# Kernel optimization log

Hardware: AMD Instinct MI355X
Metric: run time of the kernel (lower is better)

Reference implementation:

```python
import jax, jax.numpy as jnp
import numpy as np

D = 384      # d_model
NH = 8       # num_heads
HW = 96      # spatial h = w
RATIOS = (4, 8, 16)


def _p2i(x):
    # (hg wg b) c h w -> b c (hg h) (wg w), hg=wg=2, b=1
    f, c, h, w = x.shape
    return x.reshape(2, 2, c, h, w).transpose(2, 0, 3, 1, 4).reshape(1, c, 2 * h, 2 * w)


def _i2p(x):
    # b c (hg h) (wg w) -> (hg wg b) c h w, hg=wg=2, b=1
    _, c, H2, W2 = x.shape
    h, w = H2 // 2, W2 // 2
    return x.reshape(c, 2, h, 2, w).transpose(1, 3, 0, 2, 4).reshape(4, c, h, w)


def _ln(x, g, b, eps=1e-5):
    m = x.mean(-1, keepdims=True)
    v = ((x - m) ** 2).mean(-1, keepdims=True)
    return (x - m) * jax.lax.rsqrt(v + eps) * g + b


def setup_inputs() -> dict:
    key = jax.random.key(0)
    ks = jax.random.split(key, 8)
    rn = lambda k, s: jax.random.normal(k, s, dtype=jnp.float32) * 0.02
    return {
        "x": jax.random.normal(ks[0], (5, D, HW, HW), dtype=jnp.float32),
        "sal_w": rn(ks[1], (1, D)),
        "sal_b": jnp.zeros((1,), jnp.float32),
        "attn_in_w": rn(ks[2], (4, 3 * D, D)),
        "attn_in_b": jnp.zeros((4, 3 * D), jnp.float32),
        "attn_out_w": rn(ks[3], (4, D, D)),
        "attn_out_b": jnp.zeros((4, D), jnp.float32),
        "w3": rn(ks[4], (2 * D, D)),
        "b3": jnp.zeros((2 * D,), jnp.float32),
        "w4": rn(ks[5], (D, 2 * D)),
        "b4": jnp.zeros((D,), jnp.float32),
        "g1": jnp.ones((D,), jnp.float32),
        "be1": jnp.zeros((D,), jnp.float32),
        "g2": jnp.ones((D,), jnp.float32),
        "be2": jnp.zeros((D,), jnp.float32),
    }


def reference(x, sal_w, sal_b, attn_in_w, attn_in_b, attn_out_w, attn_out_b,
              w3, b3, w4, b4, g1, be1, g2, be2):
    b, c, h, w = x.shape
    loc, glb = x[:4], x[4:5]                      # (4,c,h,w), (1,c,h,w)
    pg = _i2p(glb)                                # (4,c,h/2,w/2)

    tam = jax.nn.sigmoid(jnp.einsum('oc,chw->ohw', sal_w, glb[0]) + sal_b[:, None, None])  # (1,h,w)
    tam_up = jnp.repeat(jnp.repeat(tam, 2, axis=1), 2, axis=2)[None]                        # (1,1,2h,2w)
    loc = loc * _i2p(tam_up)                      # (4,c,h,w) * (4,1,h,w)

    # multi-ratio adaptive average pooling of patched global (sizes divide exactly)
    pools = []
    for r in RATIOS:
        th, tw = round(h / r), round(w / r)
        kh, kw = (h // 2) // th, (w // 2) // tw
        p = pg.reshape(4, c, th, kh, tw, kw).mean((3, 5))
        pools.append(p.reshape(4, c, th * tw))
    kv = jnp.concatenate(pools, axis=2).transpose(0, 2, 1)   # (4,S,c)

    q = loc.reshape(4, c, h * w).transpose(0, 2, 1)          # (4,L,c)

    # 4 independent MHA blocks, vectorized over the patch dim n
    dh = c // NH
    wq, wk, wv = attn_in_w[:, :c], attn_in_w[:, c:2 * c], attn_in_w[:, 2 * c:]
    bq, bk, bv = attn_in_b[:, :c], attn_in_b[:, c:2 * c], attn_in_b[:, 2 * c:]
    heads = lambda t: t.reshape(4, -1, NH, dh).transpose(0, 2, 1, 3)
    qh = heads(jnp.einsum('nlc,ndc->nld', q, wq) + bq[:, None, :])
    kh = heads(jnp.einsum('nsc,ndc->nsd', kv, wk) + bk[:, None, :])
    vh = heads(jnp.einsum('nsc,ndc->nsd', kv, wv) + bv[:, None, :])
    scores = jnp.einsum('nhld,nhsd->nhls', qh, kh) / jnp.sqrt(jnp.float32(dh))
    attn = jax.nn.softmax(scores, axis=-1)
    ao = jnp.einsum('nhls,nhsd->nhld', attn, vh).transpose(0, 2, 1, 3).reshape(4, -1, c)
    ao = jnp.einsum('nlc,ndc->nld', ao, attn_out_w) + attn_out_b[:, None, :]  # (4,L,c)
    outputs = ao.transpose(1, 0, 2)                                           # (L,4,c)

    # residual + FFN block (dropouts are identity in eval)
    src = loc.reshape(4, c, -1).transpose(2, 0, 1) + outputs                  # (L,4,c)
    src = _ln(src, g1, be1)
    hid = jax.nn.gelu(jnp.einsum('lnc,dc->lnd', src, w3) + b3, approximate=False)
    ff = jnp.einsum('lnd,cd->lnc', hid, w4) + b4
    src = _ln(src + ff, g2, be2)
    src = src.transpose(1, 2, 0).reshape(4, c, h, w)

    # nearest-downsample (factor 2) of stitched patches, add to global
    glb = glb + _p2i(src)[:, :, ::2, ::2]
    return jnp.concatenate([src, glb], axis=0)
```

## Files before the change

### kernel.cpp

```cpp
#include <hip/hip_runtime.h>

typedef __attribute__((ext_vector_type(8))) __bf16 bf16x8;
typedef __attribute__((ext_vector_type(4))) __bf16 bf16x4;
typedef __attribute__((ext_vector_type(4))) float f32x4;

__device__ __forceinline__ bf16x8 zero8() {
  bf16x8 z;
#pragma unroll
  for (int i = 0; i < 8; ++i) z[i] = (__bf16)0.f;
  return z;
}

__device__ __forceinline__ float wave_sum(float v) {
#pragma unroll
  for (int off = 1; off < 64; off <<= 1) v += __shfl_xor(v, off);
  return v;
}

__global__ __launch_bounds__(256) void k_cvt4(const float* __restrict__ a,
    const float* __restrict__ b, const float* __restrict__ c, const float* __restrict__ d,
    __bf16* __restrict__ oa, __bf16* __restrict__ ob, __bf16* __restrict__ oc,
    __bf16* __restrict__ od) {
  const int i = blockIdx.x * 256 + threadIdx.x;
  const float* src; __bf16* dst; int off;
  if (i < 442368)      { src = a; dst = oa; off = i; }
  else if (i < 589824) { src = b; dst = ob; off = i - 442368; }
  else if (i < 663552) { src = c; dst = oc; off = i - 589824; }
  else if (i < 737280) { src = d; dst = od; off = i - 663552; }
  else return;
  const f32x4 v = ((const f32x4*)src)[off];
  bf16x4 o;
#pragma unroll
  for (int e = 0; e < 4; ++e) o[e] = (__bf16)v[e];
  ((bf16x4*)dst)[off] = o;
}

__global__ __launch_bounds__(256) void k_tam(const float* __restrict__ x,
    const float* __restrict__ sal_w, const float* __restrict__ sal_b,
    float* __restrict__ tam) {
  const int lane = threadIdx.x & 63, w = threadIdx.x >> 6;
  const int pix = blockIdx.x * 64 + lane;
  const float* g = x + (size_t)4 * 384 * 9216;
  float acc = 0.f;
  for (int c = w * 96; c < w * 96 + 96; ++c)
    acc += sal_w[c] * g[(size_t)c * 9216 + pix];
  __shared__ float part[4][64];
  part[w][lane] = acc;
  __syncthreads();
  if (w == 0) {
    float v = part[0][lane] + part[1][lane] + part[2][lane] + part[3][lane] + sal_b[0];
    tam[pix] = 1.f / (1.f + __expf(-v));
  }
}

__global__ __launch_bounds__(256) void k_locscale(const float* __restrict__ x,
    const float* __restrict__ tam, __bf16* __restrict__ Q) {
  const int n = blockIdx.y;
  const int l0 = blockIdx.x * 64;
  const int tid = threadIdx.x;
  __shared__ float tile[64][69];
  const size_t bx = (size_t)n * 384 * 9216;
  const int a = n >> 1, b = n & 1;
  for (int c0 = 0; c0 < 384; c0 += 64) {
    if (c0) __syncthreads();
#pragma unroll
    for (int pass = 0; pass < 4; ++pass) {
      int cc = pass * 16 + (tid >> 4);
      int ll = (tid & 15) * 4;
      f32x4 v = *(const f32x4*)&x[bx + (size_t)(c0 + cc) * 9216 + l0 + ll];
#pragma unroll
      for (int e = 0; e < 4; ++e) tile[cc][ll + e] = v[e];
    }
    __syncthreads();
    const int ll = tid >> 2, c1 = (tid & 3) * 16;
    const int l = l0 + ll, i = l / 96, j = l % 96;
    const float tv = tam[(a * 48 + (i >> 1)) * 96 + b * 48 + (j >> 1)];
    const size_t orow = ((size_t)n * 9216 + l) * 384 + c0 + c1;
#pragma unroll
    for (int cc = 0; cc < 16; ++cc)
      Q[orow + cc] = (__bf16)(tile[c1 + cc][ll] * tv);
  }
}

__global__ __launch_bounds__(64) void k_pool(const float* __restrict__ x,
    __bf16* __restrict__ KV) {
  const int c = blockIdx.x, n = blockIdx.y;
  const int a = n >> 1, b = n & 1;
  const float* g = x + (size_t)(4 * 384 + c) * 9216;
  __shared__ float quad[48][48];
  const int t = threadIdx.x;
  for (int k = t; k < 2304; k += 64) {
    int i = k / 48, j = k % 48;
    quad[i][j] = g[(a * 48 + i) * 96 + b * 48 + j];
  }
  __syncthreads();
  for (int s = t; s < 768; s += 64) {
    float val = 0.f;
    if (s < 576) {
      int ti = s / 24, tj = s % 24;
#pragma unroll
      for (int di = 0; di < 2; ++di)
#pragma unroll
        for (int dj = 0; dj < 2; ++dj) val += quad[ti * 2 + di][tj * 2 + dj];
      val *= 0.25f;
    } else if (s < 720) {
      int q = s - 576; int ti = q / 12, tj = q % 12;
      for (int di = 0; di < 4; ++di)
        for (int dj = 0; dj < 4; ++dj) val += quad[ti * 4 + di][tj * 4 + dj];
      val *= (1.f / 16.f);
    } else if (s < 756) {
      int q = s - 720; int ti = q / 6, tj = q % 6;
      for (int di = 0; di < 8; ++di)
        for (int dj = 0; dj < 8; ++dj) val += quad[ti * 8 + di][tj * 8 + dj];
      val *= (1.f / 64.f);
    }
    KV[((size_t)n * 768 + s) * 384 + c] = (__bf16)val;
  }
}

template <int GELU>
__global__ __launch_bounds__(256) void k_gemm(const __bf16* __restrict__ A,
    const __bf16* __restrict__ B, const float* __restrict__ bias,
    __bf16* __restrict__ C, int K, long sA, long sB, long sBias, long sC,
    float scale) {
  const int z = blockIdx.z;
  A += (size_t)z * sA; B += (size_t)z * sB; bias += (size_t)z * sBias; C += (size_t)z * sC;
  const int m0 = blockIdx.y * 128, n0 = blockIdx.x * 128;
  const int N = gridDim.x * 128;
  __shared__ __bf16 As[128 * 64], Bs[128 * 64];
  const int tid = threadIdx.x, lane = tid & 63, w = tid >> 6;
  const int wm = w >> 1, wn = w & 1;
  const int li = lane & 15, gq = lane >> 4;
  const int lrow = lane >> 3, lcol = (lane & 7) * 8;
  f32x4 acc[4][4] = {};
  const int nk = K >> 6;
  for (int kt = 0; kt < nk; ++kt) {
    const int k0 = kt * 64;
#pragma unroll
    for (int i = 0; i < 4; ++i) {
      const int r0 = w * 32 + i * 8;
      const __bf16* ga = A + (size_t)(m0 + r0 + lrow) * K + k0 + lcol;
      const __bf16* gb = B + (size_t)(n0 + r0 + lrow) * K + k0 + lcol;
      __builtin_amdgcn_global_load_lds(
          (const __attribute__((address_space(1))) void*)ga,
          (__attribute__((address_space(3))) void*)&As[r0 * 64], 16, 0, 0);
      __builtin_amdgcn_global_load_lds(
          (const __attribute__((address_space(1))) void*)gb,
          (__attribute__((address_space(3))) void*)&Bs[r0 * 64], 16, 0, 0);
    }
    __syncthreads();
#pragma unroll
    for (int kk = 0; kk < 2; ++kk) {
      bf16x8 af[4], bfr[4];
#pragma unroll
      for (int f = 0; f < 4; ++f) {
        af[f] = *(const bf16x8*)&As[(wm * 64 + f * 16 + li) * 64 + kk * 32 + gq * 8];
        bfr[f] = *(const bf16x8*)&Bs[(wn * 64 + f * 16 + li) * 64 + kk * 32 + gq * 8];
      }
#pragma unroll
      for (int fm = 0; fm < 4; ++fm)
#pragma unroll
        for (int fn = 0; fn < 4; ++fn)
          acc[fm][fn] = __builtin_amdgcn_mfma_f32_16x16x32_bf16(af[fm], bfr[fn], acc[fm][fn], 0, 0, 0);
    }
    __syncthreads();
  }
  float bv[4];
#pragma unroll
  for (int fn = 0; fn < 4; ++fn) bv[fn] = bias[n0 + wn * 64 + fn * 16 + li];
#pragma unroll
  for (int fm = 0; fm < 4; ++fm) {
    const int row = m0 + wm * 64 + fm * 16 + gq * 4;
#pragma unroll
    for (int fn = 0; fn < 4; ++fn) {
      const int col = n0 + wn * 64 + fn * 16 + li;
#pragma unroll
      for (int r = 0; r < 4; ++r) {
        float v = (acc[fm][fn][r] + bv[fn]) * scale;
        if (GELU) v = 0.5f * v * (1.f + erff(v * 0.70710678118654752f));
        C[(size_t)(row + r) * N + col] = (__bf16)v;
      }
    }
  }
}

__global__ __launch_bounds__(256) void k_kmax(const __bf16* __restrict__ KVH,
    float* __restrict__ kmax) {
  const int nh = blockIdx.x, n = nh >> 3, h = nh & 7;
  const size_t bk = (size_t)n * 768 * 768 + h * 48;
  const int tid = threadIdx.x;
  float m = 0.f;
  for (int s = tid; s < 756; s += 256) {
    float a2 = 0.f;
#pragma unroll
    for (int ch = 0; ch < 6; ++ch) {
      bf16x8 kv = *(const bf16x8*)&KVH[bk + (size_t)s * 768 + ch * 8];
#pragma unroll
      for (int e = 0; e < 8; ++e) { const float f = (float)kv[e]; a2 += f * f; }
    }
    m = fmaxf(m, a2);
  }
#pragma unroll
  for (int off = 1; off < 64; off <<= 1) m = fmaxf(m, __shfl_xor(m, off));
  __shared__ float red[4];
  if ((tid & 63) == 0) red[tid >> 6] = m;
  __syncthreads();
  if (tid == 0) kmax[nh] = fmaxf(fmaxf(red[0], red[1]), fmaxf(red[2], red[3]));
}

__global__ __launch_bounds__(256) void k_vt(const __bf16* __restrict__ KVH,
    __bf16* __restrict__ VT) {
  const int nh = blockIdx.y, n = nh >> 3, h = nh & 7;
  const int s0 = blockIdx.x * 256;
  __shared__ __bf16 tile[48][264];
  const int tid = threadIdx.x;
  const size_t bv = (size_t)n * 768 * 768 + 384 + h * 48;
#pragma unroll
  for (int it = 0; it < 6; ++it) {
    const int task = tid + it * 256;
    const int s = task / 6, ch = task % 6;
    bf16x8 v = *(const bf16x8*)&KVH[bv + (size_t)(s0 + s) * 768 + ch * 8];
#pragma unroll
    for (int e = 0; e < 8; ++e) tile[ch * 8 + e][s] = v[e];
  }
  __syncthreads();
#pragma unroll
  for (int it = 0; it < 6; ++it) {
    const int task = tid + it * 256;
    const int d = task >> 5, so = (task & 31) * 8;
    bf16x8 v2 = *(const bf16x8*)&tile[d][so];
    *(bf16x8*)&VT[((size_t)nh * 48 + d) * 768 + s0 + so] = v2;
  }
}

__global__ __launch_bounds__(256) void k_attn(const __bf16* __restrict__ QH,
    const __bf16* __restrict__ KVH, const __bf16* __restrict__ VT,
    const float* __restrict__ kmax, __bf16* __restrict__ AO) {
  const int nh = blockIdx.y, n = nh >> 3, h = nh & 7;
  const int l0 = blockIdx.x * 64;
  const int tid = threadIdx.x, lane = tid & 63, w = tid >> 6;
  const int gq = lane >> 4, li = lane & 15;
  const int l0w = l0 + w * 16;
  __shared__ __bf16 Ks[64 * 64];
  __shared__ __bf16 Vs[48 * 64];
  __shared__ __bf16 P[4][16 * 68];
  __bf16* Pw = &P[w][0];
  const size_t bq = ((size_t)n * 9216) * 384 + h * 48;
  const size_t bk = (size_t)n * 768 * 768 + h * 48;
  const __bf16* vt = VT + (size_t)nh * 48 * 768;
  const int scol = 8 * ((lane & 7) ^ (lane >> 3));
  const int rsw = 8 * (li & 7);
  bf16x8 qf[2];
#pragma unroll
  for (int kk = 0; kk < 2; ++kk) {
    const int d0 = kk * 32 + gq * 8;
    qf[kk] = (d0 < 48) ? *(const bf16x8*)&QH[bq + (size_t)(l0w + li) * 384 + d0] : zero8();
  }
  float q2 = 0.f;
#pragma unroll
  for (int kk = 0; kk < 2; ++kk)
#pragma unroll
    for (int e = 0; e < 8; ++e) { const float f = (float)qf[kk][e]; q2 += f * f; }
  q2 += __shfl_xor(q2, 16);
  q2 += __shfl_xor(q2, 32);
  const float m_fix = sqrtf(q2 * kmax[nh]);
  float l_run = 0.f;
  f32x4 o[3] = {};
  for (int t = 0; t < 12; ++t) {
    const int s0 = t * 64;
    __syncthreads();
#pragma unroll
    for (int j = 0; j < 2; ++j) {
      const int rbase = w * 16 + j * 8;
      const __bf16* src = KVH + bk + (size_t)(s0 + rbase + (lane >> 3)) * 768 + scol;
      __builtin_amdgcn_global_load_lds(
          (const __attribute__((address_space(1))) void*)src,
          (__attribute__((address_space(3))) void*)&Ks[rbase * 64], 16, 0, 0);
    }
    for (int j = w; j < 6; j += 4) {
      const int rbase = j * 8;
      const __bf16* src = vt + (size_t)(rbase + (lane >> 3)) * 768 + s0 + scol;
      __builtin_amdgcn_global_load_lds(
          (const __attribute__((address_space(1))) void*)src,
          (__attribute__((address_space(3))) void*)&Vs[rbase * 64], 16, 0, 0);
    }
    __syncthreads();
    f32x4 sc[4];
#pragma unroll
    for (int st = 0; st < 4; ++st) {
      f32x4 a = {};
#pragma unroll
      for (int kk = 0; kk < 2; ++kk) {
        const bf16x8 kf = *(const bf16x8*)&Ks[(st * 16 + li) * 64 + ((kk * 32 + gq * 8) ^ rsw)];
        a = __builtin_amdgcn_mfma_f32_16x16x32_bf16(kf, qf[kk], a, 0, 0, 0);
      }
      sc[st] = a;
    }
    if (t == 11) {
#pragma unroll
      for (int st = 0; st < 4; ++st)
#pragma unroll
        for (int r = 0; r < 4; ++r)
          if (st * 16 + gq * 4 + r >= 52) sc[st][r] = -1e30f;
    }
#pragma unroll
    for (int st = 0; st < 4; ++st)
#pragma unroll
      for (int r = 0; r < 4; ++r) {
        const float p = __builtin_amdgcn_exp2f(sc[st][r] - m_fix);
        sc[st][r] = p;
        l_run += p;
      }
#pragma unroll
    for (int st = 0; st < 4; ++st) {
      bf16x4 pk;
#pragma unroll
      for (int r = 0; r < 4; ++r) pk[r] = (__bf16)sc[st][r];
      *(bf16x4*)&Pw[li * 68 + st * 16 + gq * 4] = pk;
    }
#pragma unroll
    for (int kk = 0; kk < 2; ++kk) {
      const bf16x4 plo = *(const bf16x4*)&Pw[li * 68 + kk * 32 + gq * 8];
      const bf16x4 phi = *(const bf16x4*)&Pw[li * 68 + kk * 32 + gq * 8 + 4];
      bf16x8 ap;
#pragma unroll
      for (int e = 0; e < 4; ++e) { ap[e] = plo[e]; ap[e + 4] = phi[e]; }
#pragma unroll
      for (int df = 0; df < 3; ++df) {
        const bf16x8 bv = *(const bf16x8*)&Vs[(df * 16 + li) * 64 + ((kk * 32 + gq * 8) ^ rsw)];
        o[df] = __builtin_amdgcn_mfma_f32_16x16x32_bf16(ap, bv, o[df], 0, 0, 0);
      }
    }
  }
  l_run += __shfl_xor(l_run, 16);
  l_run += __shfl_xor(l_run, 32);
  const float inv = 1.f / l_run;
  float ir[4];
#pragma unroll
  for (int r = 0; r < 4; ++r) ir[r] = __shfl(inv, gq * 4 + r, 16);
#pragma unroll
  for (int df = 0; df < 3; ++df)
#pragma unroll
    for (int r = 0; r < 4; ++r)
      AO[bq + (size_t)(l0w + gq * 4 + r) * 384 + df * 16 + li] = (__bf16)(o[df][r] * ir[r]);
}

__global__ __launch_bounds__(256) void k_ln1(const __bf16* Q,
    const __bf16* P, const float* g1, const float* b1, __bf16* S1) {
  const size_t row = (size_t)blockIdx.x * 4 + (threadIdx.x >> 6);
  const int lane = threadIdx.x & 63;
  const __bf16* q = Q + row * 384;
  const __bf16* p = P + row * 384;
  float v[6], s = 0.f;
#pragma unroll
  for (int e = 0; e < 6; ++e) {
    const int c = e * 64 + lane;
    v[e] = (float)q[c] + (float)p[c];
    s += v[e];
  }
  s = wave_sum(s);
  const float mean = s * (1.f / 384.f);
  float var = 0.f;
#pragma unroll
  for (int e = 0; e < 6; ++e) { const float d = v[e] - mean; var += d * d; }
  var = wave_sum(var) * (1.f / 384.f);
  const float rstd = rsqrtf(var + 1e-5f);
  __bf16* o = S1 + row * 384;
#pragma unroll
  for (int e = 0; e < 6; ++e) {
    const int c = e * 64 + lane;
    o[c] = (__bf16)(((v[e] - mean) * rstd) * g1[c] + b1[c]);
  }
}

__global__ __launch_bounds__(256) void k_ln2(const __bf16* __restrict__ S1,
    const __bf16* __restrict__ FF, const float* __restrict__ g2,
    const float* __restrict__ b2, float* __restrict__ out) {
  const int n = blockIdx.y, l0 = blockIdx.x * 64;
  const int tid = threadIdx.x, w = tid >> 6, lane = tid & 63;
  __shared__ __bf16 tile[64][390];
  for (int rr = 0; rr < 16; ++rr) {
    const int ll = w * 16 + rr;
    const size_t row = ((size_t)n * 9216 + l0 + ll) * 384;
    float v[6], s = 0.f;
#pragma unroll
    for (int e = 0; e < 6; ++e) {
      const int c = e * 64 + lane;
      v[e] = (float)S1[row + c] + (float)FF[row + c];
      s += v[e];
    }
    s = wave_sum(s);
    const float mean = s * (1.f / 384.f);
    float var = 0.f;
#pragma unroll
    for (int e = 0; e < 6; ++e) { const float d = v[e] - mean; var += d * d; }
    var = wave_sum(var) * (1.f / 384.f);
    const float rstd = rsqrtf(var + 1e-5f);
#pragma unroll
    for (int e = 0; e < 6; ++e) {
      const int c = e * 64 + lane;
      tile[ll][c] = (__bf16)(((v[e] - mean) * rstd) * g2[c] + b2[c]);
    }
  }
  __syncthreads();
  for (int it = 0; it < 96; ++it) {
    const int c = it * 4 + w;
    out[((size_t)n * 384 + c) * 9216 + l0 + lane] = (float)tile[lane][c];
  }
}

__global__ __launch_bounds__(256) void k_glb(const float* __restrict__ x,
    float* out) {
  const int gl = blockIdx.x * 64 + (threadIdx.x & 63);
  const int c = blockIdx.y * 4 + (threadIdx.x >> 6);
  const int y = gl / 96, xx = gl % 96;
  const int np = ((y / 48) << 1) + (xx / 48);
  const int ls = ((y % 48) * 2) * 96 + (xx % 48) * 2;
  const float v = x[(size_t)(4 * 384 + c) * 9216 + gl] +
                  out[((size_t)np * 384 + c) * 9216 + ls];
  out[(size_t)(4 * 384 + c) * 9216 + gl] = v;
}

extern "C" void kernel_launch(void* const* d_in, const int* in_sizes, int n_in,
                              void* d_out, int out_size, void* d_ws, size_t ws_size,
                              hipStream_t stream) {
  const float* x     = (const float*)d_in[0];
  const float* sal_w = (const float*)d_in[1];
  const float* sal_b = (const float*)d_in[2];
  const float* aiw   = (const float*)d_in[3];
  const float* aib   = (const float*)d_in[4];
  const float* aow   = (const float*)d_in[5];
  const float* aob   = (const float*)d_in[6];
  const float* w3    = (const float*)d_in[7];
  const float* b3    = (const float*)d_in[8];
  const float* w4    = (const float*)d_in[9];
  const float* b4    = (const float*)d_in[10];
  const float* g1    = (const float*)d_in[11];
  const float* be1   = (const float*)d_in[12];
  const float* g2    = (const float*)d_in[13];
  const float* be2   = (const float*)d_in[14];
  float* out = (float*)d_out;
  char* ws = (char*)d_ws;

  float*  tam  = (float*)(ws + 0);
  __bf16* aiwB = (__bf16*)(ws + 36864);
  __bf16* aowB = (__bf16*)(ws + 3575808);
  __bf16* w3B  = (__bf16*)(ws + 4755456);
  __bf16* w4B  = (__bf16*)(ws + 5345280);
  __bf16* KV   = (__bf16*)(ws + 5935104);
  __bf16* KVH  = (__bf16*)(ws + 8294400);
  __bf16* Q    = (__bf16*)(ws + 13012992);
  __bf16* QHb  = (__bf16*)(ws + 41324544);
  __bf16* VTg = KV;
  __bf16* AO  = (__bf16*)d_out;
  __bf16* HID = (__bf16*)d_out;
  float* kmax = (float*)((char*)d_out + 70778368);
  __bf16* P   = QHb;
  __bf16* S1  = Q;
  __bf16* FF  = QHb;

  const float qscale = 0.20823509f;

  k_cvt4<<<2880, 256, 0, stream>>>(aiw, aow, w3, w4, aiwB, aowB, w3B, w4B);

  k_tam<<<144, 256, 0, stream>>>(x, sal_w, sal_b, tam);
  k_locscale<<<dim3(144, 4), 256, 0, stream>>>(x, tam, Q);
  k_pool<<<dim3(384, 4), 64, 0, stream>>>(x, KV);

  k_gemm<0><<<dim3(6, 6, 4), 256, 0, stream>>>(KV, aiwB + 384 * 384, aib + 384, KVH,
      384, 768L * 384, 1152L * 384, 1152L, 768L * 768, 1.f);
  k_gemm<0><<<dim3(3, 72, 4), 256, 0, stream>>>(Q, aiwB, aib, QHb,
      384, 9216L * 384, 1152L * 384, 1152L, 9216L * 384, qscale);

  k_kmax<<<32, 256, 0, stream>>>(KVH, kmax);
  k_vt<<<dim3(3, 32), 256, 0, stream>>>(KVH, VTg);

  k_attn<<<dim3(144, 32), 256, 0, stream>>>(QHb, KVH, VTg, kmax, AO);

  k_gemm<0><<<dim3(3, 72, 4), 256, 0, stream>>>(AO, aowB, aob, P,
      384, 9216L * 384, 384L * 384, 384L, 9216L * 384, 1.f);

  k_ln1<<<9216, 256, 0, stream>>>(Q, P, g1, be1, S1);

  k_gemm<1><<<dim3(6, 288, 1), 256, 0, stream>>>(S1, w3B, b3, HID,
      384, 0, 0, 0, 0, 1.f);
  k_gemm<0><<<dim3(3, 288, 1), 256, 0, stream>>>(HID, w4B, b4, FF,
      768, 0, 0, 0, 0, 1.f);

  k_ln2<<<dim3(144, 4), 256, 0, stream>>>(S1, FF, g2, be2, out);
  k_glb<<<dim3(144, 96), 256, 0, stream>>>(x, out);
}
```

Measured before the change: 360.5 us.

## Fuse LayerNorms into full-row GEMM epilogues and chunk FFN through workspace

Adds a GEMM kernel where each block owns 64 full 384-column rows, so the residual add and LayerNorm run in the epilogue. This removes the separate ln1/ln2 kernels and the round trip of the out-projection and FFN outputs through global memory. The FFN is processed in two row chunks so the GELU hidden buffer fits in workspace. Attention blocks grow to 512 threads covering 128 query rows, which shares each K/V tile load across more waves. The full-row GEMM launches fewer blocks and needs a large shared-memory footprint, which may lower occupancy.

```diff
diff --git a/kernel.cpp b/kernel.cpp
--- a/kernel.cpp
+++ b/kernel.cpp
@@ -15,6 +15,12 @@
 #pragma unroll
   for (int off = 1; off < 64; off <<= 1) v += __shfl_xor(v, off);
   return v;
+}
+
+__device__ __forceinline__ void gll(const __bf16* g, __bf16* l) {
+  __builtin_amdgcn_global_load_lds(
+      (const __attribute__((address_space(1))) void*)g,
+      (__attribute__((address_space(3))) void*)l, 16, 0, 0);
 }
 
 __global__ __launch_bounds__(256) void k_cvt4(const float* __restrict__ a,
@@ -139,14 +145,8 @@
 #pragma unroll
     for (int i = 0; i < 4; ++i) {
       const int r0 = w * 32 + i * 8;
-      const __bf16* ga = A + (size_t)(m0 + r0 + lrow) * K + k0 + lcol;
-      const __bf16* gb = B + (size_t)(n0 + r0 + lrow) * K + k0 + lcol;
-      __builtin_amdgcn_global_load_lds(
-          (const __attribute__((address_space(1))) void*)ga,
-          (__attribute__((address_space(3))) void*)&As[r0 * 64], 16, 0, 0);
-      __builtin_amdgcn_global_load_lds(
-          (const __attribute__((address_space(1))) void*)gb,
-          (__attribute__((address_space(3))) void*)&Bs[r0 * 64], 16, 0, 0);
+      gll(A + (size_t)(m0 + r0 + lrow) * K + k0 + lcol, &As[r0 * 64]);
+      gll(B + (size_t)(n0 + r0 + lrow) * K + k0 + lcol, &Bs[r0 * 64]);
     }
     __syncthreads();
 #pragma unroll
@@ -180,6 +180,101 @@
         if (GELU) v = 0.5f * v * (1.f + erff(v * 0.70710678118654752f));
         C[(size_t)(row + r) * N + col] = (__bf16)v;
       }
+    }
+  }
+}
+
+template <int SM>
+__global__ __launch_bounds__(256) void k_gemm_ln(const __bf16* __restrict__ A,
+    const __bf16* __restrict__ B, const float* __restrict__ bias,
+    const __bf16* __restrict__ R, const float* __restrict__ g,
+    const float* __restrict__ be, __bf16* __restrict__ O0, float* __restrict__ O1,
+    int K, int row0, long sB, long sBias) {
+  const int m0 = blockIdx.x * 64;
+  const int nn = (row0 + m0) / 9216;
+  B += (size_t)nn * sB; bias += (size_t)nn * sBias;
+  const int tid = threadIdx.x, lane = tid & 63, w = tid >> 6;
+  const int li = lane & 15, gq = lane >> 4;
+  const int lrow = lane >> 3, lcol = (lane & 7) * 8;
+  __shared__ __align__(16) char smem[58112];
+  __bf16* As = (__bf16*)smem;
+  __bf16* Bs = (__bf16*)(smem + 8192);
+  __bf16 (*Cs)[390] = (__bf16(*)[390])(smem + 8192);
+  f32x4 acc[4][6] = {};
+  const int nk = K >> 6;
+  for (int kt = 0; kt < nk; ++kt) {
+    const int k0 = kt * 64;
+#pragma unroll
+    for (int j = 0; j < 2; ++j) {
+      const int r0 = w * 16 + j * 8;
+      gll(A + (size_t)(m0 + r0 + lrow) * K + k0 + lcol, &As[r0 * 64]);
+    }
+#pragma unroll
+    for (int j = 0; j < 12; ++j) {
+      const int r0 = (j * 4 + w) * 8;
+      gll(B + (size_t)(r0 + lrow) * K + k0 + lcol, &Bs[r0 * 64]);
+    }
+    __syncthreads();
+#pragma unroll
+    for (int kk = 0; kk < 2; ++kk) {
+      bf16x8 af[4], bfr[6];
+#pragma unroll
+      for (int f = 0; f < 4; ++f)
+        af[f] = *(const bf16x8*)&As[(f * 16 + li) * 64 + kk * 32 + gq * 8];
+#pragma unroll
+      for (int f = 0; f < 6; ++f)
+        bfr[f] = *(const bf16x8*)&Bs[(w * 96 + f * 16 + li) * 64 + kk * 32 + gq * 8];
+#pragma unroll
+      for (int fm = 0; fm < 4; ++fm)
+#pragma unroll
+        for (int fn = 0; fn < 6; ++fn)
+          acc[fm][fn] = __builtin_amdgcn_mfma_f32_16x16x32_bf16(af[fm], bfr[fn], acc[fm][fn], 0, 0, 0);
+    }
+    __syncthreads();
+  }
+  float bv[6];
+#pragma unroll
+  for (int fn = 0; fn < 6; ++fn) bv[fn] = bias[w * 96 + fn * 16 + li];
+#pragma unroll
+  for (int fm = 0; fm < 4; ++fm)
+#pragma unroll
+    for (int fn = 0; fn < 6; ++fn)
+#pragma unroll
+      for (int r = 0; r < 4; ++r)
+        Cs[fm * 16 + gq * 4 + r][w * 96 + fn * 16 + li] = (__bf16)(acc[fm][fn][r] + bv[fn]);
+  __syncthreads();
+  for (int rr = 0; rr < 16; ++rr) {
+    const int row = w * 16 + rr;
+    const size_t grow = (size_t)(row0 + m0 + row) * 384;
+    float v[6], s = 0.f;
+#pragma unroll
+    for (int e = 0; e < 6; ++e) {
+      const int c = e * 64 + lane;
+      v[e] = (float)Cs[row][c] + (float)R[grow + c];
+      s += v[e];
+    }
+    s = wave_sum(s);
+    const float mean = s * (1.f / 384.f);
+    float var = 0.f;
+#pragma unroll
+    for (int e = 0; e < 6; ++e) { const float d = v[e] - mean; var += d * d; }
+    var = wave_sum(var) * (1.f / 384.f);
+    const float rstd = rsqrtf(var + 1e-5f);
+#pragma unroll
+    for (int e = 0; e < 6; ++e) {
+      const int c = e * 64 + lane;
+      const float o = ((v[e] - mean) * rstd) * g[c] + be[c];
+      if (SM == 0) O0[grow + c] = (__bf16)o;
+      else Cs[row][c] = (__bf16)o;
+    }
+  }
+  if (SM == 1) {
+    __syncthreads();
+    const int grow0 = row0 + m0;
+    const int l0 = grow0 % 9216;
+    for (int it = 0; it < 96; ++it) {
+      const int c = it * 4 + w;
+      O1[((size_t)nn * 384 + c) * 9216 + l0 + lane] = (float)Cs[lane][c];
     }
   }
 }
@@ -233,17 +328,17 @@
   }
 }
 
-__global__ __launch_bounds__(256) void k_attn(const __bf16* __restrict__ QH,
+__global__ __launch_bounds__(512) void k_attn(const __bf16* __restrict__ QH,
     const __bf16* __restrict__ KVH, const __bf16* __restrict__ VT,
     const float* __restrict__ kmax, __bf16* __restrict__ AO) {
   const int nh = blockIdx.y, n = nh >> 3, h = nh & 7;
-  const int l0 = blockIdx.x * 64;
+  const int l0 = blockIdx.x * 128;
   const int tid = threadIdx.x, lane = tid & 63, w = tid >> 6;
   const int gq = lane >> 4, li = lane & 15;
   const int l0w = l0 + w * 16;
   __shared__ __bf16 Ks[64 * 64];
   __shared__ __bf16 Vs[48 * 64];
-  __shared__ __bf16 P[4][16 * 68];
+  __shared__ __bf16 P[8][16 * 68];
   __bf16* Pw = &P[w][0];
   const size_t bq = ((size_t)n * 9216) * 384 + h * 48;
   const size_t bk = (size_t)n * 768 * 768 + h * 48;
@@ -269,20 +364,13 @@
   for (int t = 0; t < 12; ++t) {
     const int s0 = t * 64;
     __syncthreads();
-#pragma unroll
-    for (int j = 0; j < 2; ++j) {
-      const int rbase = w * 16 + j * 8;
-      const __bf16* src = KVH + bk + (size_t)(s0 + rbase + (lane >> 3)) * 768 + scol;
-      __builtin_amdgcn_global_load_lds(
-          (const __attribute__((address_space(1))) void*)src,
-          (__attribute__((address_space(3))) void*)&Ks[rbase * 64], 16, 0, 0);
-    }
-    for (int j = w; j < 6; j += 4) {
-      const int rbase = j * 8;
-      const __bf16* src = vt + (size_t)(rbase + (lane >> 3)) * 768 + s0 + scol;
-      __builtin_amdgcn_global_load_lds(
-          (const __attribute__((address_space(1))) void*)src,
-          (__attribute__((address_space(3))) void*)&Vs[rbase * 64], 16, 0, 0);
+    {
+      const int rbase = w * 8;
+      gll(KVH + bk + (size_t)(s0 + rbase + (lane >> 3)) * 768 + scol, &Ks[rbase * 64]);
+    }
+    if (w < 6) {
+      const int rbase = w * 8;
+      gll(vt + (size_t)(rbase + (lane >> 3)) * 768 + s0 + scol, &Vs[rbase * 64]);
     }
     __syncthreads();
     f32x4 sc[4];
@@ -343,70 +431,6 @@
 #pragma unroll
     for (int r = 0; r < 4; ++r)
       AO[bq + (size_t)(l0w + gq * 4 + r) * 384 + df * 16 + li] = (__bf16)(o[df][r] * ir[r]);
-}
-
-__global__ __launch_bounds__(256) void k_ln1(const __bf16* Q,
-    const __bf16* P, const float* g1, const float* b1, __bf16* S1) {
-  const size_t row = (size_t)blockIdx.x * 4 + (threadIdx.x >> 6);
-  const int lane = threadIdx.x & 63;
-  const __bf16* q = Q + row * 384;
-  const __bf16* p = P + row * 384;
-  float v[6], s = 0.f;
-#pragma unroll
-  for (int e = 0; e < 6; ++e) {
-    const int c = e * 64 + lane;
-    v[e] = (float)q[c] + (float)p[c];
-    s += v[e];
-  }
-  s = wave_sum(s);
-  const float mean = s * (1.f / 384.f);
-  float var = 0.f;
-#pragma unroll
-  for (int e = 0; e < 6; ++e) { const float d = v[e] - mean; var += d * d; }
-  var = wave_sum(var) * (1.f / 384.f);
-  const float rstd = rsqrtf(var + 1e-5f);
-  __bf16* o = S1 + row * 384;
-#pragma unroll
-  for (int e = 0; e < 6; ++e) {
-    const int c = e * 64 + lane;
-    o[c] = (__bf16)(((v[e] - mean) * rstd) * g1[c] + b1[c]);
-  }
-}
-
-__global__ __launch_bounds__(256) void k_ln2(const __bf16* __restrict__ S1,
-    const __bf16* __restrict__ FF, const float* __restrict__ g2,
-    const float* __restrict__ b2, float* __restrict__ out) {
-  const int n = blockIdx.y, l0 = blockIdx.x * 64;
-  const int tid = threadIdx.x, w = tid >> 6, lane = tid & 63;
-  __shared__ __bf16 tile[64][390];
-  for (int rr = 0; rr < 16; ++rr) {
-    const int ll = w * 16 + rr;
-    const size_t row = ((size_t)n * 9216 + l0 + ll) * 384;
-    float v[6], s = 0.f;
-#pragma unroll
-    for (int e = 0; e < 6; ++e) {
-      const int c = e * 64 + lane;
-      v[e] = (float)S1[row + c] + (float)FF[row + c];
-      s += v[e];
-    }
-    s = wave_sum(s);
-    const float mean = s * (1.f / 384.f);
-    float var = 0.f;
-#pragma unroll
-    for (int e = 0; e < 6; ++e) { const float d = v[e] - mean; var += d * d; }
-    var = wave_sum(var) * (1.f / 384.f);
-    const float rstd = rsqrtf(var + 1e-5f);
-#pragma unroll
-    for (int e = 0; e < 6; ++e) {
-      const int c = e * 64 + lane;
-      tile[ll][c] = (__bf16)(((v[e] - mean) * rstd) * g2[c] + b2[c]);
-    }
-  }
-  __syncthreads();
-  for (int it = 0; it < 96; ++it) {
-    const int c = it * 4 + w;
-    out[((size_t)n * 384 + c) * 9216 + l0 + lane] = (float)tile[lane][c];
-  }
 }
 
 __global__ __launch_bounds__(256) void k_glb(const float* __restrict__ x,
@@ -453,11 +477,9 @@
   __bf16* QHb  = (__bf16*)(ws + 41324544);
   __bf16* VTg = KV;
   __bf16* AO  = (__bf16*)d_out;
-  __bf16* HID = (__bf16*)d_out;
   float* kmax = (float*)((char*)d_out + 70778368);
-  __bf16* P   = QHb;
   __bf16* S1  = Q;
-  __bf16* FF  = QHb;
+  __bf16* HID = QHb;
 
   const float qscale = 0.20823509f;
 
@@ -475,18 +497,17 @@
   k_kmax<<<32, 256, 0, stream>>>(KVH, kmax);
   k_vt<<<dim3(3, 32), 256, 0, stream>>>(KVH, VTg);
 
-  k_attn<<<dim3(144, 32), 256, 0, stream>>>(QHb, KVH, VTg, kmax, AO);
-
-  k_gemm<0><<<dim3(3, 72, 4), 256, 0, stream>>>(AO, aowB, aob, P,
-      384, 9216L * 384, 384L * 384, 384L, 9216L * 384, 1.f);
-
-  k_ln1<<<9216, 256, 0, stream>>>(Q, P, g1, be1, S1);
-
-  k_gemm<1><<<dim3(6, 288, 1), 256, 0, stream>>>(S1, w3B, b3, HID,
-      384, 0, 0, 0, 0, 1.f);
-  k_gemm<0><<<dim3(3, 288, 1), 256, 0, stream>>>(HID, w4B, b4, FF,
-      768, 0, 0, 0, 0, 1.f);
-
-  k_ln2<<<dim3(144, 4), 256, 0, stream>>>(S1, FF, g2, be2, out);
+  k_attn<<<dim3(72, 32), 512, 0, stream>>>(QHb, KVH, VTg, kmax, AO);
+
+  k_gemm_ln<0><<<576, 256, 0, stream>>>(AO, aowB, aob, Q, g1, be1, S1, nullptr,
+      384, 0, 384L * 384, 384L);
+
+  for (int ch = 0; ch < 2; ++ch) {
+    k_gemm<1><<<dim3(6, 144, 1), 256, 0, stream>>>(S1 + (size_t)ch * 18432 * 384, w3B, b3,
+        HID, 384, 0, 0, 0, 0, 1.f);
+    k_gemm_ln<1><<<288, 256, 0, stream>>>(HID, w4B, b4, S1, g2, be2, nullptr, out,
+        768, ch * 18432, 0, 0);
+  }
+
   k_glb<<<dim3(144, 96), 256, 0, stream>>>(x, out);
 }
```

After: 383.8 us. 1.06x slower.
